# Performance work log

Measured on AMD Instinct MI355X. Metric: run time of the kernel, lower is better.

The kernel has to match this reference:

```python
import jax, jax.numpy as jnp
import numpy as np

NUM_EXPERTS = 64


def setup_inputs() -> dict:
    key = jax.random.key(0)
    k1, k2 = jax.random.split(key)
    x = jax.random.normal(k1, (4, 4096, 2048), dtype=jnp.float32)
    # nn.Linear default init scale ~ 1/sqrt(dim); exact init irrelevant for correctness
    gate_w = jax.random.normal(k2, (NUM_EXPERTS, 2048), dtype=jnp.float32) * (1.0 / np.sqrt(2048.0))
    expert_bias = jnp.zeros((NUM_EXPERTS,), dtype=jnp.float32)
    return {"x": x, "gate_w": gate_w, "expert_bias": expert_bias, "top_k": 8}


def reference(x, gate_w, expert_bias, top_k):
    # x: [B, S, D]; gate_w: [E, D]; expert_bias: [E]
    B, S, D = x.shape
    x_flat = x.reshape(-1, D)                                  # [T, D], T = B*S
    logits = jnp.einsum('td,ed->te', x_flat, gate_w) + expert_bias  # [T, E]
    top_k_logits, top_k_indices = jax.lax.top_k(logits, top_k)      # [T, K]
    top_k_weights = jax.nn.softmax(top_k_logits, axis=-1)           # [T, K]
    # training-mode load counting (scatter_add over expert ids)
    expert_counts = jax.ops.segment_sum(
        jnp.ones((B * S * top_k,), dtype=jnp.float32),
        top_k_indices.reshape(-1),
        num_segments=NUM_EXPERTS,
    )                                                               # [E]
    return top_k_indices, top_k_weights, expert_counts
```

## Files before the change

### kernel.cpp

```cpp
#include <hip/hip_runtime.h>
#include <math.h>

#define T_TOKENS 16384
#define D_DIM    2048
#define E_EXP    64
#define TOPK     8


#define TT   64
#define KC   64
#define XS   69
#define GS   68

__global__ __launch_bounds__(256, 4) void moe_logits_kernel(
    const float* __restrict__ x, const float* __restrict__ gw,
    float* __restrict__ part, float* __restrict__ counts_zero, int ns)
{
  __shared__ float xl[TT * XS];
  __shared__ float gl[KC * GS];

  const int tid  = threadIdx.x;
  const int ks   = blockIdx.y;
  const int tok0 = blockIdx.x * TT;
  const int ksz  = D_DIM / ns;
  const int k0   = ks * ksz;
  const int nchunk = ksz / KC;

  if (blockIdx.x == 0 && ks == 0 && tid < E_EXP) counts_zero[tid] = 0.0f;

  const int sf4 = tid & 15;
  const int str = tid >> 4;
  const int sge = tid >> 2;
  const int sgk = tid & 3;

  const int tg = tid & 15;
  const int eg = tid >> 4;

  float4 acc[4];
  #pragma unroll
  for (int j = 0; j < 4; ++j) acc[j] = make_float4(0.f, 0.f, 0.f, 0.f);

  #pragma unroll 1
  for (int c = 0; c < nchunk; ++c) {
    const int kc0 = k0 + c * KC;

    #pragma unroll
    for (int r = 0; r < 4; ++r) {
      const int t = str + 16 * r;
      float4 v = *(const float4*)&x[(size_t)(tok0 + t) * D_DIM + kc0 + sf4 * 4];
      xl[t * XS + sf4 * 4 + 0] = v.x;
      xl[t * XS + sf4 * 4 + 1] = v.y;
      xl[t * XS + sf4 * 4 + 2] = v.z;
      xl[t * XS + sf4 * 4 + 3] = v.w;
    }
    #pragma unroll
    for (int j4 = 0; j4 < 4; ++j4) {
      const int kk = sgk * 16 + j4 * 4;
      float4 v = *(const float4*)&gw[(size_t)sge * D_DIM + kc0 + kk];
      gl[(kk + 0) * GS + sge] = v.x;
      gl[(kk + 1) * GS + sge] = v.y;
      gl[(kk + 2) * GS + sge] = v.z;
      gl[(kk + 3) * GS + sge] = v.w;
    }
    __syncthreads();

    #pragma unroll 4
    for (int k = 0; k < KC; ++k) {
      float4 g = *(const float4*)&gl[k * GS + eg * 4];
      float x0 = xl[(tg * 4 + 0) * XS + k];
      float x1 = xl[(tg * 4 + 1) * XS + k];
      float x2 = xl[(tg * 4 + 2) * XS + k];
      float x3 = xl[(tg * 4 + 3) * XS + k];
      acc[0].x = fmaf(x0, g.x, acc[0].x); acc[0].y = fmaf(x0, g.y, acc[0].y);
      acc[0].z = fmaf(x0, g.z, acc[0].z); acc[0].w = fmaf(x0, g.w, acc[0].w);
      acc[1].x = fmaf(x1, g.x, acc[1].x); acc[1].y = fmaf(x1, g.y, acc[1].y);
      acc[1].z = fmaf(x1, g.z, acc[1].z); acc[1].w = fmaf(x1, g.w, acc[1].w);
      acc[2].x = fmaf(x2, g.x, acc[2].x); acc[2].y = fmaf(x2, g.y, acc[2].y);
      acc[2].z = fmaf(x2, g.z, acc[2].z); acc[2].w = fmaf(x2, g.w, acc[2].w);
      acc[3].x = fmaf(x3, g.x, acc[3].x); acc[3].y = fmaf(x3, g.y, acc[3].y);
      acc[3].z = fmaf(x3, g.z, acc[3].z); acc[3].w = fmaf(x3, g.w, acc[3].w);
    }
    __syncthreads();
  }

  #pragma unroll
  for (int j = 0; j < 4; ++j) {
    const size_t t = (size_t)tok0 + tg * 4 + j;
    *(float4*)&part[((size_t)ks * T_TOKENS + t) * E_EXP + eg * 4] = acc[j];
  }
}

__global__ __launch_bounds__(256) void topk_kernel(
    const float* __restrict__ part, const float* __restrict__ bias,
    float* __restrict__ out, int ns)
{
  __shared__ unsigned hist[E_EXP];
  const int tid = threadIdx.x;
  const int t = blockIdx.x * 256 + tid;
  if (tid < E_EXP) hist[tid] = 0;
  __syncthreads();

  float l[E_EXP];
  #pragma unroll
  for (int j = 0; j < E_EXP / 4; ++j) {
    float4 b = *(const float4*)&bias[j * 4];
    l[4*j] = b.x; l[4*j+1] = b.y; l[4*j+2] = b.z; l[4*j+3] = b.w;
  }
  for (int ks = 0; ks < ns; ++ks) {
    const float4* p = (const float4*)&part[((size_t)ks * T_TOKENS + t) * E_EXP];
    #pragma unroll
    for (int j = 0; j < E_EXP / 4; ++j) {
      float4 v = p[j];
      l[4*j] += v.x; l[4*j+1] += v.y; l[4*j+2] += v.z; l[4*j+3] += v.w;
    }
  }

  float tv[TOPK]; int tix[TOPK];
  unsigned long long used = 0ull;
  #pragma unroll
  for (int k = 0; k < TOPK; ++k) {
    float best = -INFINITY; int bi = 0;
    #pragma unroll
    for (int j = 0; j < E_EXP; ++j) {
      bool ok = (((used >> j) & 1ull) == 0ull) && (l[j] > best);
      best = ok ? l[j] : best;
      bi   = ok ? j : bi;
    }
    tv[k] = best; tix[k] = bi;
    used |= (1ull << bi);
  }

  float m = tv[0], s = 0.0f, w[TOPK];
  #pragma unroll
  for (int k = 0; k < TOPK; ++k) { w[k] = expf(tv[k] - m); s += w[k]; }
  float inv = 1.0f / s;

  #pragma unroll
  for (int k = 0; k < TOPK; ++k) {
    out[(size_t)t * TOPK + k] = (float)tix[k];
    out[(size_t)T_TOKENS * TOPK + (size_t)t * TOPK + k] = w[k] * inv;
  }

  #pragma unroll
  for (int k = 0; k < TOPK; ++k) atomicAdd(&hist[tix[k]], 1u);
  __syncthreads();
  if (tid < E_EXP)
    atomicAdd(&out[2 * (size_t)T_TOKENS * TOPK + tid], (float)hist[tid]);
}

extern "C" void kernel_launch(void* const* d_in, const int* in_sizes, int n_in,
                              void* d_out, int out_size, void* d_ws, size_t ws_size,
                              hipStream_t stream) {
  const float* x    = (const float*)d_in[0];
  const float* gw   = (const float*)d_in[1];
  const float* bias = (const float*)d_in[2];
  float* out  = (float*)d_out;
  float* part = (float*)d_ws;

  const size_t slice_bytes = (size_t)T_TOKENS * E_EXP * sizeof(float);
  int ns = 1;
  if (ws_size >= 4 * slice_bytes)      ns = 4;
  else if (ws_size >= 2 * slice_bytes) ns = 2;

  moe_logits_kernel<<<dim3(T_TOKENS / TT, ns), dim3(256), 0, stream>>>(
      x, gw, part, out + 2 * (size_t)T_TOKENS * TOPK, ns);
  topk_kernel<<<dim3(T_TOKENS / 256), dim3(256), 0, stream>>>(part, bias, out, ns);
}
```

Measured before the change: 246.6 us.

## Read gate weights as wave-uniform scalar loads and keep x rows in registers

The shared-memory staging of the gate weight tile is removed. Each wave now owns 16 experts selected through a readfirstlane-uniform base, so gate weights can be fetched with scalar (SMEM) loads. Each lane loads its own token's 64-wide x chunk from LDS into registers and accumulates 16 expert dot products. This cuts LDS traffic and bank conflicts, but uses 64 registers for x plus 16 accumulators, which may lower occupancy, and the scalar loads of weights could stall.

```diff
diff --git a/kernel.cpp b/kernel.cpp
--- a/kernel.cpp
+++ b/kernel.cpp
@@ -9,17 +9,17 @@
 
 #define TT   64
 #define KC   64
-#define XS   69
-#define GS   68
+#define XS   65
 
 __global__ __launch_bounds__(256, 4) void moe_logits_kernel(
     const float* __restrict__ x, const float* __restrict__ gw,
     float* __restrict__ part, float* __restrict__ counts_zero, int ns)
 {
   __shared__ float xl[TT * XS];
-  __shared__ float gl[KC * GS];
 
   const int tid  = threadIdx.x;
+  const int lane = tid & 63;
+  const int e_base = __builtin_amdgcn_readfirstlane(tid >> 6) * 16;
   const int ks   = blockIdx.y;
   const int tok0 = blockIdx.x * TT;
   const int ksz  = D_DIM / ns;
@@ -28,66 +28,46 @@
 
   if (blockIdx.x == 0 && ks == 0 && tid < E_EXP) counts_zero[tid] = 0.0f;
 
-  const int sf4 = tid & 15;
-  const int str = tid >> 4;
-  const int sge = tid >> 2;
-  const int sgk = tid & 3;
+  const int srow = tid >> 4;
+  const int sc4  = tid & 15;
 
-  const int tg = tid & 15;
-  const int eg = tid >> 4;
-
-  float4 acc[4];
+  float acc[16];
   #pragma unroll
-  for (int j = 0; j < 4; ++j) acc[j] = make_float4(0.f, 0.f, 0.f, 0.f);
+  for (int e = 0; e < 16; ++e) acc[e] = 0.0f;
 
   #pragma unroll 1
   for (int c = 0; c < nchunk; ++c) {
     const int kc0 = k0 + c * KC;
 
     #pragma unroll
-    for (int r = 0; r < 4; ++r) {
-      const int t = str + 16 * r;
-      float4 v = *(const float4*)&x[(size_t)(tok0 + t) * D_DIM + kc0 + sf4 * 4];
-      xl[t * XS + sf4 * 4 + 0] = v.x;
-      xl[t * XS + sf4 * 4 + 1] = v.y;
-      xl[t * XS + sf4 * 4 + 2] = v.z;
-      xl[t * XS + sf4 * 4 + 3] = v.w;
-    }
-    #pragma unroll
-    for (int j4 = 0; j4 < 4; ++j4) {
-      const int kk = sgk * 16 + j4 * 4;
-      float4 v = *(const float4*)&gw[(size_t)sge * D_DIM + kc0 + kk];
-      gl[(kk + 0) * GS + sge] = v.x;
-      gl[(kk + 1) * GS + sge] = v.y;
-      gl[(kk + 2) * GS + sge] = v.z;
-      gl[(kk + 3) * GS + sge] = v.w;
+    for (int p = 0; p < 4; ++p) {
+      const int row = srow + 16 * p;
+      float4 v = *(const float4*)&x[(size_t)(tok0 + row) * D_DIM + kc0 + sc4 * 4];
+      float* d = &xl[row * XS + sc4 * 4];
+      d[0] = v.x; d[1] = v.y; d[2] = v.z; d[3] = v.w;
     }
     __syncthreads();
 
-    #pragma unroll 4
-    for (int k = 0; k < KC; ++k) {
-      float4 g = *(const float4*)&gl[k * GS + eg * 4];
-      float x0 = xl[(tg * 4 + 0) * XS + k];
-      float x1 = xl[(tg * 4 + 1) * XS + k];
-      float x2 = xl[(tg * 4 + 2) * XS + k];
-      float x3 = xl[(tg * 4 + 3) * XS + k];
-      acc[0].x = fmaf(x0, g.x, acc[0].x); acc[0].y = fmaf(x0, g.y, acc[0].y);
-      acc[0].z = fmaf(x0, g.z, acc[0].z); acc[0].w = fmaf(x0, g.w, acc[0].w);
-      acc[1].x = fmaf(x1, g.x, acc[1].x); acc[1].y = fmaf(x1, g.y, acc[1].y);
-      acc[1].z = fmaf(x1, g.z, acc[1].z); acc[1].w = fmaf(x1, g.w, acc[1].w);
-      acc[2].x = fmaf(x2, g.x, acc[2].x); acc[2].y = fmaf(x2, g.y, acc[2].y);
-      acc[2].z = fmaf(x2, g.z, acc[2].z); acc[2].w = fmaf(x2, g.w, acc[2].w);
-      acc[3].x = fmaf(x3, g.x, acc[3].x); acc[3].y = fmaf(x3, g.y, acc[3].y);
-      acc[3].z = fmaf(x3, g.z, acc[3].z); acc[3].w = fmaf(x3, g.w, acc[3].w);
+    float xr[KC];
+    #pragma unroll
+    for (int k = 0; k < KC; ++k) xr[k] = xl[lane * XS + k];
+
+    const float* gp0 = gw + (size_t)e_base * D_DIM + kc0;
+    #pragma unroll
+    for (int e = 0; e < 16; ++e) {
+      const float* gp = gp0 + (size_t)e * D_DIM;
+      float s = acc[e];
+      #pragma unroll
+      for (int k = 0; k < KC; ++k) s = fmaf(gp[k], xr[k], s);
+      acc[e] = s;
     }
     __syncthreads();
   }
 
+  float* pp = &part[((size_t)ks * T_TOKENS + tok0 + lane) * E_EXP + e_base];
   #pragma unroll
-  for (int j = 0; j < 4; ++j) {
-    const size_t t = (size_t)tok0 + tg * 4 + j;
-    *(float4*)&part[((size_t)ks * T_TOKENS + t) * E_EXP + eg * 4] = acc[j];
-  }
+  for (int j = 0; j < 4; ++j)
+    *(float4*)&pp[4 * j] = make_float4(acc[4*j], acc[4*j+1], acc[4*j+2], acc[4*j+3]);
 }
 
 __global__ __launch_bounds__(256) void topk_kernel(
```

Result: slower. 345.8 us (+40.2%).
